# Performance work log

Hardware: AMD Instinct MI355X
Metric: run time of the kernel (lower is better)

## Reference

```python
import jax, jax.numpy as jnp
import numpy as np

N_NODES = 50000


def _sage_conv(x, src, dst, Wl, bl, Wr):
    # PyG SAGEConv (mean aggr): out = lin_l(mean_{j in N(i)} x_j) + lin_r(x_i)
    msgs = x[src]                                              # [E, F]
    agg = jax.ops.segment_sum(msgs, dst, num_segments=N_NODES)  # [N, F]
    cnt = jax.ops.segment_sum(jnp.ones((dst.shape[0],), x.dtype), dst,
                              num_segments=N_NODES)
    mean = agg / jnp.maximum(cnt, 1.0)[:, None]
    return mean @ Wl + bl + x @ Wr


def setup_inputs() -> dict:
    key = jax.random.key(0)
    ks = jax.random.split(key, 12)
    in_c, hid_c, out_c = 128, 128, 64
    E, P = 800000, 200000
    s = lambda k, shp: jax.random.normal(k, shp, dtype=jnp.float32) * (1.0 / np.sqrt(shp[0]))
    return {
        "x": jax.random.normal(ks[0], (N_NODES, in_c), dtype=jnp.float32),
        "edge_index": jax.random.randint(ks[1], (2, E), 0, N_NODES),
        "edge_pairs": jax.random.randint(ks[2], (2, P), 0, N_NODES),
        "W1l": s(ks[3], (in_c, hid_c)),
        "b1": jnp.zeros((hid_c,), jnp.float32),
        "W1r": s(ks[4], (in_c, hid_c)),
        "W2l": s(ks[5], (hid_c, out_c)),
        "b2": jnp.zeros((out_c,), jnp.float32),
        "W2r": s(ks[6], (hid_c, out_c)),
        "Wlin": s(ks[7], (2 * out_c, 1)),
        "blin": jnp.zeros((1,), jnp.float32),
    }


def reference(x, edge_index, edge_pairs, W1l, b1, W1r, W2l, b2, W2r, Wlin, blin):
    src, dst = edge_index[0], edge_index[1]
    h = jax.nn.relu(_sage_conv(x, src, dst, W1l, b1, W1r))
    z = _sage_conv(h, src, dst, W2l, b2, W2r)                 # [N, out_c]
    ps, pd = edge_pairs[0], edge_pairs[1]
    hcat = jnp.concatenate([z[ps], z[pd]], axis=1)            # [P, 2*out_c]
    logits = hcat @ Wlin + blin                               # [P, 1]
    return jax.nn.sigmoid(logits).reshape(-1)
```

## Files before the change

### kernel.cpp

```cpp
#include <hip/hip_runtime.h>
#include <math.h>


typedef __attribute__((ext_vector_type(8))) short bf16x8;
typedef __attribute__((ext_vector_type(4))) float f32x4;
typedef unsigned int uint32;
typedef unsigned short ushort16;

#define MAXBUCK 784
#define NHB 512
#define SLABB 2048

__device__ __forceinline__ ushort16 f2bf(float f) {
    uint32 u = __float_as_uint(f);
    uint32 r = u + 0x7FFFu + ((u >> 16) & 1u);
    return (ushort16)(r >> 16);
}


__global__ __launch_bounds__(256)
void prep_kernel(const float* __restrict__ x, uint32* __restrict__ xh, long long n4,
                 const float* __restrict__ W1l, const float* __restrict__ W1r,
                 ushort16* __restrict__ W1t,
                 const float* __restrict__ W2l, const float* __restrict__ W2r,
                 const float* __restrict__ Wlin, const float* __restrict__ b2,
                 float* __restrict__ fw, float* __restrict__ fc,
                 const int* __restrict__ dst, int* __restrict__ hcnt, int E,
                 int nbx, int nbw1) {
    __shared__ int lh[MAXBUCK];
    int b = blockIdx.x;
    int t = threadIdx.x;
    if (b < nbx) {
        long long i = (long long)b * 256 + t;
        if (i < n4) {
            float4 v = ((const float4*)x)[i];
            uint2 o;
            o.x = (uint32)f2bf(v.x) | ((uint32)f2bf(v.y) << 16);
            o.y = (uint32)f2bf(v.z) | ((uint32)f2bf(v.w) << 16);
            ((uint2*)xh)[i] = o;
        }
    } else if (b < nbx + nbw1) {
        int idx = (b - nbx) * 256 + t;
        int n = idx >> 8, k = idx & 255;
        float v = (k < 128) ? W1l[k * 128 + n] : W1r[(k - 128) * 128 + n];
        W1t[idx ^ ((n & 7) << 3)] = f2bf(v);
    } else if (b == nbx + nbw1) {
        if (t < 128) {
            float a = 0.f, c = 0.f;
            for (int l = 0; l < 64; ++l) {
                float w = W2l[t * 64 + l];
                a += w * Wlin[l];
                c += w * Wlin[64 + l];
            }
            fw[t] = a; fw[128 + t] = c;
        } else {
            int k = t - 128;
            float a = 0.f, c = 0.f;
            for (int l = 0; l < 64; ++l) {
                float w = W2r[k * 64 + l];
                a += w * Wlin[l];
                c += w * Wlin[64 + l];
            }
            fw[256 + k] = a; fw[384 + k] = c;
        }
        if (t == 0) { float s = 0.f; for (int l = 0; l < 64; ++l) s += b2[l] * Wlin[l];      fc[0] = s; }
        if (t == 1) { float s = 0.f; for (int l = 0; l < 64; ++l) s += b2[l] * Wlin[64 + l]; fc[1] = s; }
    } else {
        int hb = b - nbx - nbw1 - 1;
        for (int i = t; i < MAXBUCK; i += 256) lh[i] = 0;
        __syncthreads();
        int per = (E + NHB - 1) / NHB;
        int e0 = hb * per, e1 = min(e0 + per, E);
        for (int e = e0 + t; e < e1; e += 256) atomicAdd(&lh[dst[e] >> 6], 1);
        __syncthreads();
        for (int i = t; i < MAXBUCK; i += 256)
            hcnt[hb * MAXBUCK + i] = lh[i];
    }
}


__global__ __launch_bounds__(256)
void offs_kernel(const int* __restrict__ hcnt, int* __restrict__ boff,
                 int* __restrict__ tot) {
    int k = blockIdx.x * 4 + (threadIdx.x >> 6);
    int lane = threadIdx.x & 63;
    if (k >= MAXBUCK) return;
    int carry = 0;
    #pragma unroll
    for (int c = 0; c < NHB / 64; ++c) {
        int hb = c * 64 + lane;
        int v = hcnt[hb * MAXBUCK + k];
        int s = v;
        #pragma unroll
        for (int off = 1; off < 64; off <<= 1) {
            int u = __shfl_up(s, off, 64);
            if (lane >= off) s += u;
        }
        boff[hb * MAXBUCK + k] = carry + s - v;
        carry += __shfl(s, 63, 64);
    }
    if (lane == 0) tot[k] = carry;
}


__global__ __launch_bounds__(256)
void scatter_kernel(const int* __restrict__ src, const int* __restrict__ dst,
                    const int* __restrict__ boff,
                    uint32* __restrict__ recs, int E) {
    __shared__ int lh[MAXBUCK];
    __shared__ int lb[MAXBUCK];
    int t = threadIdx.x;
    int hb = blockIdx.x;
    int per = (E + NHB - 1) / NHB;
    int e0 = hb * per, e1 = min(e0 + per, E);
    for (int i = t; i < MAXBUCK; i += 256) {
        lh[i] = 0;
        lb[i] = i * SLABB + boff[hb * MAXBUCK + i];
    }
    __syncthreads();
    for (int e = e0 + t; e < e1; e += 256) {
        int d = dst[e];
        int bk = d >> 6;
        int r = atomicAdd(&lh[bk], 1);
        int p = lb[bk] + r;
        if (p < (bk + 1) * SLABB)
            recs[p] = (uint32)src[e] | ((uint32)(d & 63) << 16);
    }
}


__global__ __launch_bounds__(512, 8)
void sortagg_kernel(const uint32* __restrict__ xh,
                    const uint32* __restrict__ recs, const int* __restrict__ tot,
                    int2* __restrict__ rowse, ushort16* __restrict__ esrc_g,
                    uint32* __restrict__ meanh, int N) {
    __shared__ int lh[64];
    __shared__ int st_[64];
    __shared__ unsigned short es[SLABB];
    int b = blockIdx.x;
    int t = threadIdx.x;
    int s0 = b * SLABB;
    int cntb = tot[b]; if (cntb > SLABB) cntb = SLABB;
    int s1 = s0 + cntb;
    if (t < 64) lh[t] = 0;
    __syncthreads();
    for (int i = s0 + t; i < s1; i += 512)
        atomicAdd(&lh[recs[i] >> 16], 1);
    __syncthreads();
    if (t < 64) {
        int v = lh[t];
        int incl = v;
        #pragma unroll
        for (int off = 1; off < 64; off <<= 1) {
            int u = __shfl_up(incl, off, 64);
            if (t >= off) incl += u;
        }
        int excl = incl - v;
        int node = b * 64 + t;
        if (node < N) rowse[node] = make_int2(s0 + excl, v);
        st_[t] = excl;
        lh[t] = excl;
    }
    __syncthreads();
    for (int i = s0 + t; i < s1; i += 512) {
        uint32 r = recs[i];
        int pos = atomicAdd(&lh[r >> 16], 1);
        unsigned short sv = (unsigned short)(r & 0xFFFFu);
        es[pos] = sv;
        ((unsigned short*)esrc_g)[s0 + pos] = sv;
    }
    __syncthreads();

    int wave = t >> 6, lane = t & 63;
    int q = lane >> 4;
    int w = lane & 15;
    for (int rr = 0; rr < 8; ++rr) {
        int n = wave * 8 + rr;
        int node = b * 64 + n;
        if (node >= N) break;
        int e0 = st_[n], e1 = lh[n];
        if (e0 == e1) {
            if (q == 0) ((uint4*)meanh)[(size_t)node * 16 + w] = make_uint4(0u, 0u, 0u, 0u);
            continue;
        }
        float acc[8] = {};
        for (int k = e0; k < e1; k += 16) {
            int idx[4]; float msk[4];
            #pragma unroll
            for (int j = 0; j < 4; ++j) {
                int e = k + q * 4 + j;
                int valid = e < e1;
                idx[j] = es[valid ? e : e0];
                msk[j] = valid ? 1.f : 0.f;
            }
            #pragma unroll
            for (int j = 0; j < 4; ++j) {
                uint4 v = ((const uint4*)xh)[(size_t)idx[j] * 16 + w];
                acc[0] += __uint_as_float(v.x << 16) * msk[j];
                acc[1] += __uint_as_float(v.x & 0xFFFF0000u) * msk[j];
                acc[2] += __uint_as_float(v.y << 16) * msk[j];
                acc[3] += __uint_as_float(v.y & 0xFFFF0000u) * msk[j];
                acc[4] += __uint_as_float(v.z << 16) * msk[j];
                acc[5] += __uint_as_float(v.z & 0xFFFF0000u) * msk[j];
                acc[6] += __uint_as_float(v.w << 16) * msk[j];
                acc[7] += __uint_as_float(v.w & 0xFFFF0000u) * msk[j];
            }
        }
        #pragma unroll
        for (int i = 0; i < 8; ++i) {
            acc[i] += __shfl_xor(acc[i], 16, 64);
            acc[i] += __shfl_xor(acc[i], 32, 64);
        }
        if (q == 0) {
            float inv = 1.0f / (float)(e1 - e0);
            uint4 o;
            o.x = (uint32)f2bf(acc[0] * inv) | ((uint32)f2bf(acc[1] * inv) << 16);
            o.y = (uint32)f2bf(acc[2] * inv) | ((uint32)f2bf(acc[3] * inv) << 16);
            o.z = (uint32)f2bf(acc[4] * inv) | ((uint32)f2bf(acc[5] * inv) << 16);
            o.w = (uint32)f2bf(acc[6] * inv) | ((uint32)f2bf(acc[7] * inv) << 16);
            ((uint4*)meanh)[(size_t)node * 16 + w] = o;
        }
    }
}


__global__ __launch_bounds__(256)
void gemm1_mfma_kernel(const ushort16* __restrict__ meanh,
                       const ushort16* __restrict__ xh,
                       const ushort16* __restrict__ W1t,
                       const float* __restrict__ b1,
                       const float* __restrict__ fw,
                       float2* __restrict__ pab, float2* __restrict__ quv, int N) {
    __shared__ uint4 w1s[4096];
    for (int u = threadIdx.x; u < 4096; u += 256)
        w1s[u] = ((const uint4*)W1t)[u];
    __syncthreads();
    int wave = threadIdx.x >> 6;
    int lane = threadIdx.x & 63;
    int m = lane & 15;
    int quad = lane >> 4;
    int row0 = blockIdx.x * 128 + wave * 32;
    int ar0 = row0 + m;      if (ar0 > N - 1) ar0 = N - 1;
    int ar1 = row0 + 16 + m; if (ar1 > N - 1) ar1 = N - 1;
    const char* wbase = (const char*)w1s;
    f32x4 acc[2][8];
    #pragma unroll
    for (int h = 0; h < 2; ++h)
        #pragma unroll
        for (int c = 0; c < 8; ++c) acc[h][c] = (f32x4){0.f, 0.f, 0.f, 0.f};
    #pragma unroll
    for (int ks = 0; ks < 8; ++ks) {
        int k0 = ks * 32;
        const ushort16* Ab = (ks < 4) ? meanh : xh;
        bf16x8 a0 = *(const bf16x8*)(Ab + (size_t)ar0 * 128 + (k0 & 127) + quad * 8);
        bf16x8 a1 = *(const bf16x8*)(Ab + (size_t)ar1 * 128 + (k0 & 127) + quad * 8);
        #pragma unroll
        for (int c = 0; c < 8; ++c) {
            int boff_ = (((c * 16 + m) << 9) + ((k0 + quad * 8) << 1)) ^ ((m & 7) << 4);
            bf16x8 bfr = *(const bf16x8*)(wbase + boff_);
            acc[0][c] = __builtin_amdgcn_mfma_f32_16x16x32_bf16(a0, bfr, acc[0][c], 0, 0, 0);
            acc[1][c] = __builtin_amdgcn_mfma_f32_16x16x32_bf16(a1, bfr, acc[1][c], 0, 0, 0);
        }
    }
    float da[2][4] = {}, dc[2][4] = {}, db[2][4] = {}, dd[2][4] = {};
    #pragma unroll
    for (int c = 0; c < 8; ++c) {
        int col = c * 16 + m;
        float bias = b1[col];
        float wa = fw[col], wc = fw[128 + col], wb = fw[256 + col], wd = fw[384 + col];
        #pragma unroll
        for (int h = 0; h < 2; ++h) {
            #pragma unroll
            for (int r = 0; r < 4; ++r) {
                float v = fmaxf(acc[h][c][r] + bias, 0.f);
                da[h][r] += v * wa; dc[h][r] += v * wc;
                db[h][r] += v * wb; dd[h][r] += v * wd;
            }
        }
    }
    #pragma unroll
    for (int h = 0; h < 2; ++h) {
        #pragma unroll
        for (int r = 0; r < 4; ++r) {
            #pragma unroll
            for (int msk = 1; msk < 16; msk <<= 1) {
                da[h][r] += __shfl_xor(da[h][r], msk, 64);
                dc[h][r] += __shfl_xor(dc[h][r], msk, 64);
                db[h][r] += __shfl_xor(db[h][r], msk, 64);
                dd[h][r] += __shfl_xor(dd[h][r], msk, 64);
            }
        }
    }
    if (m == 0) {
        #pragma unroll
        for (int h = 0; h < 2; ++h) {
            #pragma unroll
            for (int r = 0; r < 4; ++r) {
                int grow = row0 + h * 16 + quad * 4 + r;
                if (grow < N) {
                    pab[grow] = make_float2(da[h][r], dc[h][r]);
                    quv[grow] = make_float2(db[h][r], dd[h][r]);
                }
            }
        }
    }
}


__global__ __launch_bounds__(256)
void agg_link_kernel(const float2* __restrict__ pab,
                     const float2* __restrict__ quv,
                     const int2* __restrict__ rowse,
                     const ushort16* __restrict__ esrc,
                     const float* __restrict__ fc,
                     float* __restrict__ za, float* __restrict__ zb, int N) {
    int gi = blockIdx.x * blockDim.x + threadIdx.x;
    int i = gi >> 2;
    int q = gi & 3;
    if (i >= N) return;
    int2 se = rowse[i];
    int s0 = se.x, s1 = se.x + se.y;
    float a[4] = {}, c[4] = {};
    for (int k = s0 + q; k < s1; k += 16) {
        int idx[4]; float mk[4];
        #pragma unroll
        for (int j = 0; j < 4; ++j) {
            int kk = k + j * 4;
            int v = kk < s1;
            idx[j] = esrc[v ? kk : k];
            mk[j] = v ? 1.f : 0.f;
        }
        #pragma unroll
        for (int j = 0; j < 4; ++j) {
            float2 p = pab[idx[j]];
            a[j] += p.x * mk[j];
            c[j] += p.y * mk[j];
        }
    }
    float spa = (a[0] + a[1]) + (a[2] + a[3]);
    float spc = (c[0] + c[1]) + (c[2] + c[3]);
    spa += __shfl_xor(spa, 1, 64); spa += __shfl_xor(spa, 2, 64);
    spc += __shfl_xor(spc, 1, 64); spc += __shfl_xor(spc, 2, 64);
    if (q == 0) {
        float inv = (se.y > 0) ? 1.0f / (float)se.y : 0.f;
        float2 qv = quv[i];
        za[i] = spa * inv + qv.x + fc[0];
        zb[i] = spc * inv + qv.y + fc[1];
    }
}


__global__ void link_kernel(const float* __restrict__ za, const float* __restrict__ zb,
                            const int* __restrict__ ps, const int* __restrict__ pd,
                            const float* __restrict__ blin,
                            float* __restrict__ out, int P) {
    int p = blockIdx.x * blockDim.x + threadIdx.x;
    if (p >= P) return;
    float logit = za[ps[p]] + zb[pd[p]] + blin[0];
    out[p] = 1.0f / (1.0f + expf(-logit));
}


extern "C" void kernel_launch(void* const* d_in, const int* in_sizes, int n_in,
                              void* d_out, int out_size, void* d_ws, size_t ws_size,
                              hipStream_t stream) {
    const float* x          = (const float*)d_in[0];
    const int*   edge_index = (const int*)d_in[1];
    const int*   edge_pairs = (const int*)d_in[2];
    const float* W1l        = (const float*)d_in[3];
    const float* b1         = (const float*)d_in[4];
    const float* W1r        = (const float*)d_in[5];
    const float* W2l        = (const float*)d_in[6];
    const float* b2         = (const float*)d_in[7];
    const float* W2r        = (const float*)d_in[8];
    const float* Wlin       = (const float*)d_in[9];
    const float* blin       = (const float*)d_in[10];
    float* out = (float*)d_out;

    const int N = in_sizes[0] / 128;
    const int E = in_sizes[1] / 2;
    const int P = in_sizes[2] / 2;
    const int NBUCK = (N + 63) >> 6;

    const int* src = edge_index;
    const int* dst = edge_index + E;
    const int* ps  = edge_pairs;
    const int* pd  = edge_pairs + P;

    ushort16* xh    = (ushort16*)d_ws;
    ushort16* meanh = xh + (size_t)N * 128;
    ushort16* W1t   = meanh + (size_t)N * 128;
    float* fw      = (float*)(W1t + 128 * 256);
    float* fc      = fw + 512;
    float2* pab    = (float2*)(fc + 16);
    float2* quv    = pab + N;
    float* za      = (float*)(quv + N);
    float* zb      = za + N;
    int2* rowse    = (int2*)(zb + N);
    int* tot       = (int*)(rowse + N);
    int* hcnt      = tot + MAXBUCK;
    int* boff      = hcnt + NHB * MAXBUCK;
    uint32* recs   = (uint32*)(boff + NHB * MAXBUCK);
    ushort16* esrc = (ushort16*)(recs + (size_t)MAXBUCK * SLABB);

    const long long n4 = (long long)N * 128 / 4;
    const int nbx  = (int)((n4 + 255) / 256);
    const int nbw1 = 128;

    prep_kernel<<<nbx + nbw1 + 1 + NHB, 256, 0, stream>>>(
        x, (uint32*)xh, n4, W1l, W1r, W1t, W2l, W2r, Wlin, b2, fw, fc,
        dst, hcnt, E, nbx, nbw1);

    offs_kernel<<<MAXBUCK / 4, 256, 0, stream>>>(hcnt, boff, tot);
    scatter_kernel<<<NHB, 256, 0, stream>>>(src, dst, boff, recs, E);

    sortagg_kernel<<<NBUCK, 512, 0, stream>>>((const uint32*)xh, recs, tot,
                                              rowse, esrc, (uint32*)meanh, N);

    gemm1_mfma_kernel<<<(N + 127) / 128, 256, 0, stream>>>(meanh, xh, W1t, b1, fw,
                                                           pab, quv, N);

    agg_link_kernel<<<(4 * N + 255) / 256, 256, 0, stream>>>(pab, quv, rowse, esrc, fc,
                                                             za, zb, N);

    link_kernel<<<(P + 255) / 256, 256, 0, stream>>>(za, zb, ps, pd, blin, out, P);
}
```

Measured before the change: 176.2 us.

## Software-pipeline neighbor gathers across nodes in sortagg kernel

Restructures the per-wave aggregation loop into a flattened stream of 16-edge chunks across the wave's 8 nodes, issuing the next chunk's global gathers before accumulating the current one. This double-buffers loads to hide gather latency and removes per-node loop boundaries. Launch bounds drop from 8 to 4 waves per SIMD to allow the extra registers, which may reduce occupancy.

```diff
diff --git a/kernel.cpp b/kernel.cpp
--- a/kernel.cpp
+++ b/kernel.cpp
@@ -129,7 +129,34 @@
 }
 
 
-__global__ __launch_bounds__(512, 8)
+#define GATHER_ISSUE(V0, V1, V2, V3, M0, M1, M2, M3)                         \
+    do {                                                                     \
+        int eb_ = kk + q * 4;                                                \
+        int v0_ = (eb_ + 0) < e1c; int i0_ = es[v0_ ? (eb_ + 0) : e0c];      \
+        int v1_ = (eb_ + 1) < e1c; int i1_ = es[v1_ ? (eb_ + 1) : e0c];      \
+        int v2_ = (eb_ + 2) < e1c; int i2_ = es[v2_ ? (eb_ + 2) : e0c];      \
+        int v3_ = (eb_ + 3) < e1c; int i3_ = es[v3_ ? (eb_ + 3) : e0c];      \
+        M0 = v0_ ? 1.f : 0.f; M1 = v1_ ? 1.f : 0.f;                          \
+        M2 = v2_ ? 1.f : 0.f; M3 = v3_ ? 1.f : 0.f;                          \
+        V0 = xh4[(size_t)i0_ * 16 + w];                                      \
+        V1 = xh4[(size_t)i1_ * 16 + w];                                      \
+        V2 = xh4[(size_t)i2_ * 16 + w];                                      \
+        V3 = xh4[(size_t)i3_ * 16 + w];                                      \
+    } while (0)
+
+#define GATHER_ACC(V, M)                                                     \
+    do {                                                                     \
+        acc0 += __uint_as_float(V.x << 16) * M;                              \
+        acc1 += __uint_as_float(V.x & 0xFFFF0000u) * M;                      \
+        acc2 += __uint_as_float(V.y << 16) * M;                              \
+        acc3 += __uint_as_float(V.y & 0xFFFF0000u) * M;                      \
+        acc4 += __uint_as_float(V.z << 16) * M;                              \
+        acc5 += __uint_as_float(V.z & 0xFFFF0000u) * M;                      \
+        acc6 += __uint_as_float(V.w << 16) * M;                              \
+        acc7 += __uint_as_float(V.w & 0xFFFF0000u) * M;                      \
+    } while (0)
+
+__global__ __launch_bounds__(512, 4)
 void sortagg_kernel(const uint32* __restrict__ xh,
                     const uint32* __restrict__ recs, const int* __restrict__ tot,
                     int2* __restrict__ rowse, ushort16* __restrict__ esrc_g,
@@ -171,55 +198,77 @@
     }
     __syncthreads();
 
+    const uint4* xh4 = (const uint4*)xh;
     int wave = t >> 6, lane = t & 63;
     int q = lane >> 4;
     int w = lane & 15;
+    int nbase = wave * 8;
+
     for (int rr = 0; rr < 8; ++rr) {
-        int n = wave * 8 + rr;
+        int n = nbase + rr;
         int node = b * 64 + n;
-        if (node >= N) break;
-        int e0 = st_[n], e1 = lh[n];
-        if (e0 == e1) {
-            if (q == 0) ((uint4*)meanh)[(size_t)node * 16 + w] = make_uint4(0u, 0u, 0u, 0u);
-            continue;
-        }
-        float acc[8] = {};
-        for (int k = e0; k < e1; k += 16) {
-            int idx[4]; float msk[4];
-            #pragma unroll
-            for (int j = 0; j < 4; ++j) {
-                int e = k + q * 4 + j;
-                int valid = e < e1;
-                idx[j] = es[valid ? e : e0];
-                msk[j] = valid ? 1.f : 0.f;
-            }
-            #pragma unroll
-            for (int j = 0; j < 4; ++j) {
-                uint4 v = ((const uint4*)xh)[(size_t)idx[j] * 16 + w];
-                acc[0] += __uint_as_float(v.x << 16) * msk[j];
-                acc[1] += __uint_as_float(v.x & 0xFFFF0000u) * msk[j];
-                acc[2] += __uint_as_float(v.y << 16) * msk[j];
-                acc[3] += __uint_as_float(v.y & 0xFFFF0000u) * msk[j];
-                acc[4] += __uint_as_float(v.z << 16) * msk[j];
-                acc[5] += __uint_as_float(v.z & 0xFFFF0000u) * msk[j];
-                acc[6] += __uint_as_float(v.w << 16) * msk[j];
-                acc[7] += __uint_as_float(v.w & 0xFFFF0000u) * msk[j];
-            }
-        }
-        #pragma unroll
-        for (int i = 0; i < 8; ++i) {
-            acc[i] += __shfl_xor(acc[i], 16, 64);
-            acc[i] += __shfl_xor(acc[i], 32, 64);
-        }
-        if (q == 0) {
-            float inv = 1.0f / (float)(e1 - e0);
-            uint4 o;
-            o.x = (uint32)f2bf(acc[0] * inv) | ((uint32)f2bf(acc[1] * inv) << 16);
-            o.y = (uint32)f2bf(acc[2] * inv) | ((uint32)f2bf(acc[3] * inv) << 16);
-            o.z = (uint32)f2bf(acc[4] * inv) | ((uint32)f2bf(acc[5] * inv) << 16);
-            o.w = (uint32)f2bf(acc[6] * inv) | ((uint32)f2bf(acc[7] * inv) << 16);
-            ((uint4*)meanh)[(size_t)node * 16 + w] = o;
-        }
+        if (node < N && st_[n] == lh[n] && q == 0)
+            ((uint4*)meanh)[(size_t)node * 16 + w] = make_uint4(0u, 0u, 0u, 0u);
+    }
+
+    int ln = -1;
+    int kk = 0, e0c = 0, e1c = 0;
+    auto ADV = [&]() -> bool {
+        if (ln >= 0 && kk + 16 < e1c) { kk += 16; return true; }
+        for (++ln; ln < 8; ++ln) {
+            int nn = nbase + ln;
+            int a = st_[nn], bb = lh[nn];
+            if (a < bb) { kk = a; e0c = a; e1c = bb; return true; }
+        }
+        return false;
+    };
+
+    float acc0 = 0.f, acc1 = 0.f, acc2 = 0.f, acc3 = 0.f;
+    float acc4 = 0.f, acc5 = 0.f, acc6 = 0.f, acc7 = 0.f;
+    uint4 a0 = {}, a1 = {}, a2 = {}, a3 = {};
+    float m0 = 0.f, m1 = 0.f, m2 = 0.f, m3 = 0.f;
+    int cln = 0, ce0 = 0, ce1 = 0; bool clast = false;
+
+    bool have = ADV();
+    if (have) {
+        cln = ln; ce0 = e0c; ce1 = e1c; clast = (kk + 16 >= e1c);
+        GATHER_ISSUE(a0, a1, a2, a3, m0, m1, m2, m3);
+    }
+    while (have) {
+        int pln = cln, pe0 = ce0, pe1 = ce1; bool plast = clast;
+        uint4 b0 = {}, b1 = {}, b2 = {}, b3 = {};
+        float n0 = 0.f, n1 = 0.f, n2 = 0.f, n3 = 0.f;
+        bool hnext = ADV();
+        if (hnext) {
+            cln = ln; ce0 = e0c; ce1 = e1c; clast = (kk + 16 >= e1c);
+            GATHER_ISSUE(b0, b1, b2, b3, n0, n1, n2, n3);
+        }
+        GATHER_ACC(a0, m0); GATHER_ACC(a1, m1);
+        GATHER_ACC(a2, m2); GATHER_ACC(a3, m3);
+        if (plast) {
+            acc0 += __shfl_xor(acc0, 16, 64); acc0 += __shfl_xor(acc0, 32, 64);
+            acc1 += __shfl_xor(acc1, 16, 64); acc1 += __shfl_xor(acc1, 32, 64);
+            acc2 += __shfl_xor(acc2, 16, 64); acc2 += __shfl_xor(acc2, 32, 64);
+            acc3 += __shfl_xor(acc3, 16, 64); acc3 += __shfl_xor(acc3, 32, 64);
+            acc4 += __shfl_xor(acc4, 16, 64); acc4 += __shfl_xor(acc4, 32, 64);
+            acc5 += __shfl_xor(acc5, 16, 64); acc5 += __shfl_xor(acc5, 32, 64);
+            acc6 += __shfl_xor(acc6, 16, 64); acc6 += __shfl_xor(acc6, 32, 64);
+            acc7 += __shfl_xor(acc7, 16, 64); acc7 += __shfl_xor(acc7, 32, 64);
+            int node = b * 64 + nbase + pln;
+            if (q == 0 && node < N) {
+                float inv = 1.0f / (float)(pe1 - pe0);
+                uint4 o;
+                o.x = (uint32)f2bf(acc0 * inv) | ((uint32)f2bf(acc1 * inv) << 16);
+                o.y = (uint32)f2bf(acc2 * inv) | ((uint32)f2bf(acc3 * inv) << 16);
+                o.z = (uint32)f2bf(acc4 * inv) | ((uint32)f2bf(acc5 * inv) << 16);
+                o.w = (uint32)f2bf(acc6 * inv) | ((uint32)f2bf(acc7 * inv) << 16);
+                ((uint4*)meanh)[(size_t)node * 16 + w] = o;
+            }
+            acc0 = acc1 = acc2 = acc3 = acc4 = acc5 = acc6 = acc7 = 0.f;
+        }
+        a0 = b0; a1 = b1; a2 = b2; a3 = b3;
+        m0 = n0; m1 = n1; m2 = n2; m3 = n3;
+        have = hnext;
     }
 }
 
```

Measured after the change: 180.5 us. +2.4%, slower.
